# Kernel tuning notes

Measured on AMD Instinct MI355X. Metric: run time of the kernel, lower is better.

Reference implementation:

```python
import jax, jax.numpy as jnp
import numpy as np

B, S, D, E, TOPK = 4, 2048, 1024, 8, 2


def setup_inputs() -> dict:
    key = jax.random.key(0)
    k1, k2, k3 = jax.random.split(key, 3)
    scale = 1.0 / np.sqrt(D)
    return {
        "x": jax.random.normal(k1, (B, S, D), dtype=jnp.float32),
        "gate_w": jax.random.normal(k2, (D, E), dtype=jnp.float32) * scale,
        "gate_b": jnp.zeros((E,), dtype=jnp.float32),
        "expert_w": jax.random.normal(k3, (E, D, D), dtype=jnp.float32) * scale,
        "expert_b": jnp.zeros((E, D), dtype=jnp.float32),
        "top_k": TOPK,
    }


def reference(x, gate_w, gate_b, expert_w, expert_b, top_k):
    # Gating: softmax over experts, then top-k expert indices per token.
    logits = x @ gate_w + gate_b                      # [B, S, E]
    probs = jax.nn.softmax(logits, axis=-1)
    _, top_idx = jax.lax.top_k(probs, top_k)          # [B, S, top_k]
    # Binary membership mask (original multiplies by mask, NOT gate probs).
    mask = jax.nn.one_hot(top_idx, probs.shape[-1], dtype=x.dtype).sum(axis=-2)  # [B, S, E]
    # Dense per-expert linear on all tokens (as in the original loop).
    expert_out = jnp.einsum('bsd,edf->bsef', x, expert_w) + expert_b  # [B, S, E, D]
    # Mask-multiply-accumulate over experts.
    return jnp.einsum('bse,bsef->bsf', mask, expert_out)             # [B, S, D]
```

## Files before the change

### kernel.cpp

```cpp
#include <hip/hip_runtime.h>
#include <stdint.h>

#define T_TOK 8192
#define DD    1024
#define EN    8
#define CPAD  16

#define BM 128
#define BN 128
#define BK 64
#define NT (DD / BK)
#define NWG 4096

#define GATE_NB 512

#define AS1 __attribute__((address_space(1)))
#define AS3 __attribute__((address_space(3)))

typedef __bf16 v8bf __attribute__((ext_vector_type(8)));
typedef float  v4f  __attribute__((ext_vector_type(4)));

__device__ __forceinline__ uint16_t f2b(float f) {
  uint32_t u = __builtin_bit_cast(uint32_t, f);
  u += 0x7FFFu + ((u >> 16) & 1u);
  return (uint16_t)(u >> 16);
}
__device__ __forceinline__ float b2f(uint16_t h) {
  uint32_t u = (uint32_t)h << 16;
  return __builtin_bit_cast(float, u);
}

template <bool WRITE_PIDX>
__global__ __launch_bounds__(256) void prep_kernel(
    const float* __restrict__ x, const float* __restrict__ gw,
    const float* __restrict__ gb, uint16_t* __restrict__ xb,
    int* __restrict__ counts, int* __restrict__ lists, int* __restrict__ pidx,
    const float* __restrict__ w, uint16_t* __restrict__ wt) {
  extern __shared__ __align__(16) uint8_t smem[];
  const int bid = blockIdx.x;
  const int tid = threadIdx.x;

  if (bid >= GATE_NB) {
    float (*tile)[65] = (float(*)[65])smem;
    const int tb = bid - GATE_NB;
    const int e = tb >> 8;
    const int rem = tb & 255;
    const int f0 = (rem & 15) * 64, d0 = (rem >> 4) * 64;
    const float* wsrc = w + ((size_t)e << 20);
    uint16_t* wdst = wt + ((size_t)e << 20);
    const int r4 = tid >> 4;
    const int c4 = (tid & 15) * 4;
#pragma unroll
    for (int i = 0; i < 4; ++i) {
      int row = i * 16 + r4;
      const float4 v = *(const float4*)(wsrc + (size_t)(d0 + row) * DD + f0 + c4);
      tile[row][c4 + 0] = v.x; tile[row][c4 + 1] = v.y;
      tile[row][c4 + 2] = v.z; tile[row][c4 + 3] = v.w;
    }
    __syncthreads();
#pragma unroll
    for (int i = 0; i < 4; ++i) {
      int f = i * 16 + r4;
      ushort4 h;
      h.x = f2b(tile[c4 + 0][f]); h.y = f2b(tile[c4 + 1][f]);
      h.z = f2b(tile[c4 + 2][f]); h.w = f2b(tile[c4 + 3][f]);
      *(ushort4*)(wdst + (size_t)(f0 + f) * DD + d0 + c4) = h;
    }
    return;
  }

  float* sgwt = (float*)smem;
  float (*sx)[DD] = (float(*)[DD])(smem + 32768);
  int* se1 = (int*)(smem + 49152);
  int* se2 = (int*)(smem + 49152 + 64);

#pragma unroll
  for (int i = 0; i < 8; ++i) {
    const int j4 = i * 256 + tid;
    const float4 v = ((const float4*)gw)[j4];
    const int d = j4 >> 1;
    const int e0 = (j4 & 1) * 4;
    sgwt[(e0 + 0) * DD + d] = v.x;
    sgwt[(e0 + 1) * DD + d] = v.y;
    sgwt[(e0 + 2) * DD + d] = v.z;
    sgwt[(e0 + 3) * DD + d] = v.w;
  }
  __syncthreads();

  const int t0 = bid * 16;
  const int wid = tid >> 6, lane = tid & 63;

  for (int r = 0; r < 4; ++r) {
    const int tt = t0 + wid * 4 + r;
    const float4* xg = (const float4*)(x + (size_t)tt * DD);
    float4* sxv = (float4*)sx[wid];
    ushort4* xbv = (ushort4*)(xb + (size_t)tt * DD);
#pragma unroll
    for (int i = 0; i < 4; ++i) {
      float4 v = xg[i * 64 + lane];
      sxv[i * 64 + lane] = v;
      ushort4 h;
      h.x = f2b(v.x); h.y = f2b(v.y); h.z = f2b(v.z); h.w = f2b(v.w);
      xbv[i * 64 + lane] = h;
    }
    asm volatile("s_waitcnt lgkmcnt(0)" ::: "memory");

    double part[8];
#pragma unroll
    for (int e = 0; e < 8; ++e) part[e] = 0.0;
#pragma unroll
    for (int c = 0; c < 16; ++c) {
      const double xd = (double)sx[wid][c * 64 + lane];
#pragma unroll
      for (int e = 0; e < 8; ++e)
        part[e] += xd * (double)sgwt[e * DD + c * 64 + lane];
    }
#pragma unroll
    for (int off = 1; off < 64; off <<= 1) {
#pragma unroll
      for (int e = 0; e < 8; ++e) part[e] += __shfl_xor(part[e], off);
    }
    if (lane == 0) {
      double lg[8];
#pragma unroll
      for (int i = 0; i < 8; ++i) lg[i] = part[i] + (double)gb[i];
      int e1 = 0; double m1 = lg[0];
#pragma unroll
      for (int i = 1; i < 8; ++i) if (lg[i] > m1) { m1 = lg[i]; e1 = i; }
      int e2 = 0; double m2 = -1.0e300;
#pragma unroll
      for (int i = 0; i < 8; ++i) if (i != e1 && lg[i] > m2) { m2 = lg[i]; e2 = i; }
      se1[wid * 4 + r] = e1;
      se2[wid * 4 + r] = e2;
    }
  }
  __syncthreads();

  if (tid < EN) {
    int cnt = 0;
#pragma unroll
    for (int i = 0; i < 16; ++i) cnt += (se1[i] == tid) + (se2[i] == tid);
    int base = atomicAdd(&counts[tid * CPAD], cnt);
    int* dst = lists + tid * T_TOK;
    for (int i = 0; i < 16; ++i) {
      if (se1[i] == tid) {
        if (WRITE_PIDX) pidx[2 * (t0 + i)] = tid * T_TOK + base;
        dst[base++] = t0 + i;
      }
      if (se2[i] == tid) {
        if (WRITE_PIDX) pidx[2 * (t0 + i) + 1] = tid * T_TOK + base;
        dst[base++] = t0 + i;
      }
    }
  }
}

template <bool ATOMIC>
__global__ __launch_bounds__(256, 2) void expert_gemm_kernel(
    const uint16_t* __restrict__ xb, const uint16_t* __restrict__ wt,
    const float* __restrict__ eb, const int* __restrict__ counts,
    const int* __restrict__ lists, uint16_t* __restrict__ dst,
    float* __restrict__ dstf) {
  const int orig = blockIdx.x;
  const int e = orig & 7;
  const int rem = orig >> 3;
  const int m0 = (rem >> 3) * BM;
  const int n0 = (rem & 7) * BN;
  const int cnt = counts[e * CPAD];
  if (m0 >= cnt) return;
  int rows = cnt - m0; if (rows > BM) rows = BM;
  int offsE = 0;
  if (!ATOMIC) {
#pragma unroll
    for (int i = 0; i < EN; ++i) offsE += (i < e) ? counts[i * CPAD] : 0;
  }

  __shared__ uint16_t sA[2 * BM * BK];
  __shared__ uint16_t sB[2 * BN * BK];
  __shared__ int toks[BM];

  const int tid = threadIdx.x;
  if (tid < BM) {
    int rr = tid < rows ? tid : 0;
    toks[tid] = lists[e * T_TOK + m0 + rr];
  }
  __syncthreads();

  const int lane = tid & 63;
  const int wid = tid >> 6;
  const int wm = wid >> 1;
  const int wn = wid & 1;

  v4f acc[4][4];
#pragma unroll
  for (int i = 0; i < 4; ++i)
#pragma unroll
    for (int j = 0; j < 4; ++j) acc[i][j] = (v4f){0.f, 0.f, 0.f, 0.f};

  const int koff = (((tid & 7) ^ ((tid >> 3) & 7)) << 3);
  const uint16_t* wte = wt + ((size_t)e << 20) + (size_t)n0 * DD;
  const uint16_t* aptr[4];
  const uint16_t* bptr[4];
#pragma unroll
  for (int i = 0; i < 4; ++i) {
    int row = i * 32 + (tid >> 3);
    aptr[i] = xb + (size_t)toks[row] * DD + koff;
    bptr[i] = wte + (size_t)row * DD + koff;
  }

#define STAGE(buf, k0)                                                          \
  {                                                                             \
    _Pragma("unroll")                                                           \
    for (int i = 0; i < 4; ++i) {                                               \
      int idx = i * 256 + tid;                                                  \
      __builtin_amdgcn_global_load_lds(                                         \
          (const AS1 uint32_t*)(aptr[i] + (k0)),                                \
          (AS3 uint32_t*)(sA + (buf) * (BM * BK) + idx * 8), 16, 0, 0);         \
      __builtin_amdgcn_global_load_lds(                                         \
          (const AS1 uint32_t*)(bptr[i] + (k0)),                                \
          (AS3 uint32_t*)(sB + (buf) * (BN * BK) + idx * 8), 16, 0, 0);         \
    }                                                                           \
  }

  const int c0 = lane >> 4;
  const int rsel = lane & 15;
  const int rx = lane & 7;

  STAGE(0, 0);
  int cur = 0;
  for (int kt = 0; kt < NT; ++kt) {
    if (kt + 1 < NT) {
      STAGE(cur ^ 1, (kt + 1) * BK);
      __builtin_amdgcn_sched_barrier(0);
      asm volatile("s_waitcnt vmcnt(8)" ::: "memory");
    } else {
      __builtin_amdgcn_sched_barrier(0);
      asm volatile("s_waitcnt vmcnt(0)" ::: "memory");
    }
    __builtin_amdgcn_sched_barrier(0);
    __builtin_amdgcn_s_barrier();
    __builtin_amdgcn_sched_barrier(0);

    const uint16_t* a_base = sA + cur * (BM * BK);
    const uint16_t* b_base = sB + cur * (BN * BK);
#pragma unroll
    for (int kk = 0; kk < 2; ++kk) {
      v8bf af[4], bfr[4];
#pragma unroll
      for (int m = 0; m < 4; ++m) {
        int row_a = wm * 64 + m * 16 + rsel;
        af[m] = *(const v8bf*)(a_base + row_a * BK + (((kk * 4 + c0) ^ rx) << 3));
      }
#pragma unroll
      for (int n = 0; n < 4; ++n) {
        int row_b = wn * 64 + n * 16 + rsel;
        bfr[n] = *(const v8bf*)(b_base + row_b * BK + (((kk * 4 + c0) ^ rx) << 3));
      }
#pragma unroll
      for (int m = 0; m < 4; ++m)
#pragma unroll
        for (int n = 0; n < 4; ++n)
          acc[m][n] = __builtin_amdgcn_mfma_f32_16x16x32_bf16(
              af[m], bfr[n], acc[m][n], 0, 0, 0);
    }
    __builtin_amdgcn_sched_barrier(0);
    __builtin_amdgcn_s_barrier();
    cur ^= 1;
  }
#undef STAGE

  const int col = lane & 15, rq = lane >> 4;
  if (!ATOMIC) {
    uint16_t* base = dst + (size_t)(offsE + m0) * DD + n0 + wn * 64 + col;
#pragma unroll
    for (int m = 0; m < 4; ++m) {
#pragma unroll
      for (int j = 0; j < 4; ++j) {
        int trow = wm * 64 + m * 16 + rq * 4 + j;
        if (trow < rows) {
          uint16_t* orow = base + (size_t)trow * DD;
#pragma unroll
          for (int n = 0; n < 4; ++n) orow[n * 16] = f2b(acc[m][n][j]);
        }
      }
    }
  } else {
    float biasv[4];
#pragma unroll
    for (int n = 0; n < 4; ++n)
      biasv[n] = eb[e * DD + n0 + wn * 64 + n * 16 + col];
#pragma unroll
    for (int m = 0; m < 4; ++m) {
#pragma unroll
      for (int j = 0; j < 4; ++j) {
        int trow = wm * 64 + m * 16 + rq * 4 + j;
        if (trow < rows) {
          float* orow = dstf + (size_t)toks[trow] * DD + n0;
#pragma unroll
          for (int n = 0; n < 4; ++n)
            atomicAdd(orow + wn * 64 + n * 16 + col, acc[m][n][j] + biasv[n]);
        }
      }
    }
  }
}

__global__ __launch_bounds__(256) void combine_kernel(
    const uint16_t* __restrict__ wsO, const int* __restrict__ pidx,
    const int* __restrict__ counts, const float* __restrict__ eb,
    float* __restrict__ out) {
  __shared__ int soff[EN];
  const int tid = threadIdx.x;
  if (tid == 0) {
    int o = 0;
#pragma unroll
    for (int i = 0; i < EN; ++i) { soff[i] = o; o += counts[i * CPAD]; }
  }
  __syncthreads();
  const int t0 = blockIdx.x * 4;
#pragma unroll
  for (int r = 0; r < 4; ++r) {
    const int t = t0 + r;
    const int pi1 = pidx[2 * t], pi2 = pidx[2 * t + 1];
    const int e1 = pi1 >> 13, p1 = pi1 & (T_TOK - 1);
    const int e2 = pi2 >> 13, p2 = pi2 & (T_TOK - 1);
    ushort4 r1 = ((const ushort4*)(wsO + (size_t)(soff[e1] + p1) * DD))[tid];
    ushort4 r2 = ((const ushort4*)(wsO + (size_t)(soff[e2] + p2) * DD))[tid];
    v4f b1 = ((const v4f*)(eb + e1 * DD))[tid];
    v4f b2 = ((const v4f*)(eb + e2 * DD))[tid];
    v4f o;
    o[0] = b2f(r1.x) + b2f(r2.x) + b1[0] + b2[0];
    o[1] = b2f(r1.y) + b2f(r2.y) + b1[1] + b2[1];
    o[2] = b2f(r1.z) + b2f(r2.z) + b1[2] + b2[2];
    o[3] = b2f(r1.w) + b2f(r2.w) + b1[3] + b2[3];
    ((v4f*)(out + (size_t)t * DD))[tid] = o;
  }
}

extern "C" void kernel_launch(void* const* d_in, const int* in_sizes, int n_in,
                              void* d_out, int out_size, void* d_ws, size_t ws_size,
                              hipStream_t stream) {
  const float* x  = (const float*)d_in[0];
  const float* gw = (const float*)d_in[1];
  const float* gb = (const float*)d_in[2];
  const float* ew = (const float*)d_in[3];
  const float* ebias = (const float*)d_in[4];
  float* out = (float*)d_out;

  uint8_t* ws = (uint8_t*)d_ws;
  int* counts = (int*)ws;
  int* lists  = (int*)(ws + 512);
  int* pidx   = (int*)(ws + 512 + 262144);
  uint16_t* xb = (uint16_t*)(ws + 512 + 262144 + 65536);
  uint16_t* wt = (uint16_t*)(ws + 512 + 262144 + 65536 + 16777216);
  uint16_t* wsO = (uint16_t*)(ws + 512 + 262144 + 65536 + 2 * 16777216);
  const size_t need = 512ull + 262144 + 65536 + 2 * 16777216 +
                      (size_t)2 * T_TOK * DD * sizeof(uint16_t);
  const bool use_ws = ws_size >= need;

  hipMemsetAsync(counts, 0, 512, stream);
  if (use_ws) {
    prep_kernel<true><<<GATE_NB + 2048, 256, 49408, stream>>>(
        x, gw, gb, xb, counts, lists, pidx, ew, wt);
    expert_gemm_kernel<false><<<NWG, 256, 0, stream>>>(
        xb, wt, ebias, counts, lists, wsO, nullptr);
    combine_kernel<<<T_TOK / 4, 256, 0, stream>>>(wsO, pidx, counts, ebias, out);
  } else {
    hipMemsetAsync(d_out, 0, (size_t)out_size * sizeof(float), stream);
    prep_kernel<false><<<GATE_NB + 2048, 256, 49408, stream>>>(
        x, gw, gb, xb, counts, lists, pidx, ew, wt);
    expert_gemm_kernel<true><<<NWG, 256, 0, stream>>>(
        xb, wt, ebias, counts, lists, nullptr, out);
  }
}
```

Measured before the change: 104.2 us.

## Enlarge expert GEMM tiles to 256x256 with 512 threads and split A/B staging

Expert GEMM tiles grow from 128x128 to 256x256 and workgroups from 256 to 512 threads. Each wave now computes 128x64 outputs, which roughly halves global and LDS traffic per FLOP. The prefetch of the next K-tile is split so A loads are issued before the first half-step of MFMAs and B loads between the two half-steps, and the MFMA blocks are wrapped in s_setprio raises. This costs more registers per wave (32 accumulator vectors), lower occupancy, and many fewer workgroups, so tail effects and load imbalance across experts' variable token counts may grow.

Result: slower. 114.8 us (+10.1%).

```diff
diff --git a/kernel.cpp b/kernel.cpp
--- a/kernel.cpp
+++ b/kernel.cpp
@@ -6,11 +6,11 @@
 #define EN    8
 #define CPAD  16
 
-#define BM 128
-#define BN 128
+#define BM 256
+#define BN 256
 #define BK 64
 #define NT (DD / BK)
-#define NWG 4096
+#define NWG 1024
 
 #define GATE_NB 512
 
@@ -156,7 +156,7 @@
 }
 
 template <bool ATOMIC>
-__global__ __launch_bounds__(256, 2) void expert_gemm_kernel(
+__global__ __launch_bounds__(512) void expert_gemm_kernel(
     const uint16_t* __restrict__ xb, const uint16_t* __restrict__ wt,
     const float* __restrict__ eb, const int* __restrict__ counts,
     const int* __restrict__ lists, uint16_t* __restrict__ dst,
@@ -164,8 +164,8 @@
   const int orig = blockIdx.x;
   const int e = orig & 7;
   const int rem = orig >> 3;
-  const int m0 = (rem >> 3) * BM;
-  const int n0 = (rem & 7) * BN;
+  const int m0 = (rem >> 2) * BM;
+  const int n0 = (rem & 3) * BN;
   const int cnt = counts[e * CPAD];
   if (m0 >= cnt) return;
   int rows = cnt - m0; if (rows > BM) rows = BM;
@@ -188,12 +188,12 @@
 
   const int lane = tid & 63;
   const int wid = tid >> 6;
-  const int wm = wid >> 1;
-  const int wn = wid & 1;
-
-  v4f acc[4][4];
-#pragma unroll
-  for (int i = 0; i < 4; ++i)
+  const int wm = wid >> 2;
+  const int wn = wid & 3;
+
+  v4f acc[8][4];
+#pragma unroll
+  for (int i = 0; i < 8; ++i)
 #pragma unroll
     for (int j = 0; j < 4; ++j) acc[i][j] = (v4f){0.f, 0.f, 0.f, 0.f};
 
@@ -203,19 +203,26 @@
   const uint16_t* bptr[4];
 #pragma unroll
   for (int i = 0; i < 4; ++i) {
-    int row = i * 32 + (tid >> 3);
+    int row = i * 64 + (tid >> 3);
     aptr[i] = xb + (size_t)toks[row] * DD + koff;
     bptr[i] = wte + (size_t)row * DD + koff;
   }
 
-#define STAGE(buf, k0)                                                          \
+#define STAGE_A(buf, k0)                                                        \
   {                                                                             \
     _Pragma("unroll")                                                           \
     for (int i = 0; i < 4; ++i) {                                               \
-      int idx = i * 256 + tid;                                                  \
+      int idx = i * 512 + tid;                                                  \
       __builtin_amdgcn_global_load_lds(                                         \
           (const AS1 uint32_t*)(aptr[i] + (k0)),                                \
           (AS3 uint32_t*)(sA + (buf) * (BM * BK) + idx * 8), 16, 0, 0);         \
+    }                                                                           \
+  }
+#define STAGE_B(buf, k0)                                                        \
+  {                                                                             \
+    _Pragma("unroll")                                                           \
+    for (int i = 0; i < 4; ++i) {                                               \
+      int idx = i * 512 + tid;                                                  \
       __builtin_amdgcn_global_load_lds(                                         \
           (const AS1 uint32_t*)(bptr[i] + (k0)),                                \
           (AS3 uint32_t*)(sB + (buf) * (BN * BK) + idx * 8), 16, 0, 0);         \
@@ -226,13 +233,17 @@
   const int rsel = lane & 15;
   const int rx = lane & 7;
 
-  STAGE(0, 0);
+  STAGE_A(0, 0);
+  STAGE_B(0, 0);
   int cur = 0;
   for (int kt = 0; kt < NT; ++kt) {
-    if (kt + 1 < NT) {
-      STAGE(cur ^ 1, (kt + 1) * BK);
+    const int k1 = (kt + 1) * BK;
+    const bool next = (kt + 1 < NT);
+
+    if (next) {
+      STAGE_A(cur ^ 1, k1);
       __builtin_amdgcn_sched_barrier(0);
-      asm volatile("s_waitcnt vmcnt(8)" ::: "memory");
+      asm volatile("s_waitcnt vmcnt(4)" ::: "memory");
     } else {
       __builtin_amdgcn_sched_barrier(0);
       asm volatile("s_waitcnt vmcnt(0)" ::: "memory");
@@ -243,40 +254,67 @@
 
     const uint16_t* a_base = sA + cur * (BM * BK);
     const uint16_t* b_base = sB + cur * (BN * BK);
-#pragma unroll
-    for (int kk = 0; kk < 2; ++kk) {
-      v8bf af[4], bfr[4];
-#pragma unroll
-      for (int m = 0; m < 4; ++m) {
-        int row_a = wm * 64 + m * 16 + rsel;
-        af[m] = *(const v8bf*)(a_base + row_a * BK + (((kk * 4 + c0) ^ rx) << 3));
+    {
+      v8bf af[8], bfr[4];
+#pragma unroll
+      for (int m = 0; m < 8; ++m) {
+        int row_a = wm * 128 + m * 16 + rsel;
+        af[m] = *(const v8bf*)(a_base + row_a * BK + ((c0 ^ rx) << 3));
       }
 #pragma unroll
       for (int n = 0; n < 4; ++n) {
         int row_b = wn * 64 + n * 16 + rsel;
-        bfr[n] = *(const v8bf*)(b_base + row_b * BK + (((kk * 4 + c0) ^ rx) << 3));
-      }
-#pragma unroll
-      for (int m = 0; m < 4; ++m)
+        bfr[n] = *(const v8bf*)(b_base + row_b * BK + ((c0 ^ rx) << 3));
+      }
+      __builtin_amdgcn_s_setprio(1);
+#pragma unroll
+      for (int m = 0; m < 8; ++m)
 #pragma unroll
         for (int n = 0; n < 4; ++n)
           acc[m][n] = __builtin_amdgcn_mfma_f32_16x16x32_bf16(
               af[m], bfr[n], acc[m][n], 0, 0, 0);
+      __builtin_amdgcn_s_setprio(0);
+    }
+
+    if (next) STAGE_B(cur ^ 1, k1);
+    __builtin_amdgcn_sched_barrier(0);
+    {
+      v8bf af[8], bfr[4];
+#pragma unroll
+      for (int m = 0; m < 8; ++m) {
+        int row_a = wm * 128 + m * 16 + rsel;
+        af[m] = *(const v8bf*)(a_base + row_a * BK + (((4 + c0) ^ rx) << 3));
+      }
+#pragma unroll
+      for (int n = 0; n < 4; ++n) {
+        int row_b = wn * 64 + n * 16 + rsel;
+        bfr[n] = *(const v8bf*)(b_base + row_b * BK + (((4 + c0) ^ rx) << 3));
+      }
+      __builtin_amdgcn_s_setprio(1);
+#pragma unroll
+      for (int m = 0; m < 8; ++m)
+#pragma unroll
+        for (int n = 0; n < 4; ++n)
+          acc[m][n] = __builtin_amdgcn_mfma_f32_16x16x32_bf16(
+              af[m], bfr[n], acc[m][n], 0, 0, 0);
+      __builtin_amdgcn_s_setprio(0);
     }
     __builtin_amdgcn_sched_barrier(0);
     __builtin_amdgcn_s_barrier();
+    __builtin_amdgcn_sched_barrier(0);
     cur ^= 1;
   }
-#undef STAGE
+#undef STAGE_A
+#undef STAGE_B
 
   const int col = lane & 15, rq = lane >> 4;
   if (!ATOMIC) {
     uint16_t* base = dst + (size_t)(offsE + m0) * DD + n0 + wn * 64 + col;
 #pragma unroll
-    for (int m = 0; m < 4; ++m) {
+    for (int m = 0; m < 8; ++m) {
 #pragma unroll
       for (int j = 0; j < 4; ++j) {
-        int trow = wm * 64 + m * 16 + rq * 4 + j;
+        int trow = wm * 128 + m * 16 + rq * 4 + j;
         if (trow < rows) {
           uint16_t* orow = base + (size_t)trow * DD;
 #pragma unroll
@@ -290,10 +328,10 @@
     for (int n = 0; n < 4; ++n)
       biasv[n] = eb[e * DD + n0 + wn * 64 + n * 16 + col];
 #pragma unroll
-    for (int m = 0; m < 4; ++m) {
+    for (int m = 0; m < 8; ++m) {
 #pragma unroll
       for (int j = 0; j < 4; ++j) {
-        int trow = wm * 64 + m * 16 + rq * 4 + j;
+        int trow = wm * 128 + m * 16 + rq * 4 + j;
         if (trow < rows) {
           float* orow = dstf + (size_t)toks[trow] * DD + n0;
 #pragma unroll
@@ -362,14 +400,14 @@
   if (use_ws) {
     prep_kernel<true><<<GATE_NB + 2048, 256, 49408, stream>>>(
         x, gw, gb, xb, counts, lists, pidx, ew, wt);
-    expert_gemm_kernel<false><<<NWG, 256, 0, stream>>>(
+    expert_gemm_kernel<false><<<NWG, 512, 0, stream>>>(
         xb, wt, ebias, counts, lists, wsO, nullptr);
     combine_kernel<<<T_TOK / 4, 256, 0, stream>>>(wsO, pidx, counts, ebias, out);
   } else {
     hipMemsetAsync(d_out, 0, (size_t)out_size * sizeof(float), stream);
     prep_kernel<false><<<GATE_NB + 2048, 256, 49408, stream>>>(
         x, gw, gb, xb, counts, lists, pidx, ew, wt);
-    expert_gemm_kernel<true><<<NWG, 256, 0, stream>>>(
+    expert_gemm_kernel<true><<<NWG, 512, 0, stream>>>(
         xb, wt, ebias, counts, lists, nullptr, out);
   }
 }
```
